# Performance work log

Hardware: AMD Instinct MI355X
Metric: run time of the kernel (lower is better)

Reference implementation:

```python
import jax, jax.numpy as jnp
import numpy as np

N, H, W = 4, 96, 96
C, G, K = 128, 8, 3
GC = C // G          # group channels = 16
P = K * K            # sampling points per group = 9
PAD = K // 2
OFS = 1.0            # offset_scale
HID = 4 * C          # mlp hidden
EPS = 1e-5           # torch nn.LayerNorm default eps


def _ln(x, g, b):
    m = jnp.mean(x, -1, keepdims=True)
    v = jnp.mean((x - m) ** 2, -1, keepdims=True)
    return (x - m) * jax.lax.rsqrt(v + EPS) * g + b


def _dcnv3_core(x, offset, mask):
    # x: (n,H,W,C) channels-last, offset: (n,H,W,G*P*2), mask: (n,H,W,G,P) softmaxed.
    # Faithful port of dcnv3_core_pytorch (stride=1, dilation=1, zero-pad grid_sample,
    # align_corners=False -> pixel = loc*size - 0.5).
    n = x.shape[0]
    xp = jnp.pad(x, ((0, 0), (PAD, PAD), (PAD, PAD), (0, 0)))
    Hin, Win = H + 2 * PAD, W + 2 * PAD
    L = H * W
    base = (K - 1) // 2 + 0.5
    ref_x = (base + jnp.arange(W, dtype=x.dtype)) / Win  # normalized by padded size
    ref_y = (base + jnp.arange(H, dtype=x.dtype)) / Hin
    k = jnp.arange(K, dtype=x.dtype) - (K - 1) // 2
    dx = jnp.repeat(k, K) / Win  # torch meshgrid('ij'): kernel-x varies slowest
    dy = jnp.tile(k, K) / Hin
    off = offset.reshape(n, H, W, G, P, 2)
    # absolute sampling pixel coords (grid_sample align_corners=False)
    px = (ref_x[None, None, :, None, None] + dx * OFS + off[..., 0] * OFS / Win) * Win - 0.5
    py = (ref_y[None, :, None, None, None] + dy * OFS + off[..., 1] * OFS / Hin) * Hin - 0.5
    # layout (n,G,L,P)
    px = px.transpose(0, 3, 1, 2, 4).reshape(n, G, L, P)
    py = py.transpose(0, 3, 1, 2, 4).reshape(n, G, L, P)
    mk = mask.transpose(0, 3, 1, 2, 4).reshape(n, G, L, P)
    xg = xp.reshape(n, Hin * Win, G, GC).transpose(0, 2, 1, 3)
    x0 = jnp.floor(px); y0 = jnp.floor(py)
    fx = px - x0; fy = py - y0
    x0 = x0.astype(jnp.int32); y0 = y0.astype(jnp.int32)
    x1 = x0 + 1; y1 = y0 + 1
    out = jnp.zeros((n, G, L, GC), x.dtype)
    for yi, xi, w in ((y0, x0, (1 - fy) * (1 - fx)), (y0, x1, (1 - fy) * fx),
                      (y1, x0, fy * (1 - fx)), (y1, x1, fy * fx)):
        valid = (yi >= 0) & (yi < Hin) & (xi >= 0) & (xi < Win)
        idx = jnp.clip(yi, 0, Hin - 1) * Win + jnp.clip(xi, 0, Win - 1)
        v = jnp.take_along_axis(xg, idx.reshape(n, G, L * P, 1), axis=2)
        v = v.reshape(n, G, L, P, GC)
        out = out + jnp.einsum('nglp,nglpc->nglc', jnp.where(valid, w, 0.0) * mk, v)
    return out.transpose(0, 2, 1, 3).reshape(n, H, W, C)


def _dcn(x, w_in, b_in, dw_k, dw_b, dwg, dwb, w_off, b_off, w_msk, b_msk, w_out, b_out):
    n = x.shape[0]
    xproj = x @ w_in + b_in
    x1 = jax.lax.conv_general_dilated(
        x, dw_k, (1, 1), 'SAME',
        dimension_numbers=('NHWC', 'HWIO', 'NHWC'),
        feature_group_count=C) + dw_b
    x1 = jax.nn.gelu(_ln(x1, dwg, dwb), approximate=False)
    offset = x1 @ w_off + b_off
    mask = jax.nn.softmax((x1 @ w_msk + b_msk).reshape(n, H, W, G, P), axis=-1)
    y = _dcnv3_core(xproj, offset, mask)
    return y @ w_out + b_out


def setup_inputs() -> dict:
    key = jax.random.key(0)
    ks = jax.random.split(key, 10)
    rn = lambda k, s, sc: jax.random.normal(k, s, jnp.float32) * sc
    return {
        'x': rn(ks[0], (N, H, W, C), 1.0),
        'ln1g': jnp.ones((C,), jnp.float32), 'ln1b': jnp.zeros((C,), jnp.float32),
        'w_in': rn(ks[1], (C, C), 0.02), 'b_in': jnp.zeros((C,), jnp.float32),
        'dw_k': rn(ks[2], (K, K, 1, C), 0.1), 'dw_b': jnp.zeros((C,), jnp.float32),
        'dwg': jnp.ones((C,), jnp.float32), 'dwb': jnp.zeros((C,), jnp.float32),
        'w_off': rn(ks[3], (C, G * P * 2), 0.01), 'b_off': rn(ks[4], (G * P * 2,), 0.1),
        'w_msk': rn(ks[5], (C, G * P), 0.02), 'b_msk': jnp.zeros((G * P,), jnp.float32),
        'w_out': rn(ks[6], (C, C), 0.02), 'b_out': jnp.zeros((C,), jnp.float32),
        'ln2g': jnp.ones((C,), jnp.float32), 'ln2b': jnp.zeros((C,), jnp.float32),
        'w1': rn(ks[7], (C, HID), 0.02), 'b1': jnp.zeros((HID,), jnp.float32),
        'w2': rn(ks[8], (HID, C), 0.02), 'b2': jnp.zeros((C,), jnp.float32),
    }


def reference(x, ln1g, ln1b, w_in, b_in, dw_k, dw_b, dwg, dwb, w_off, b_off,
              w_msk, b_msk, w_out, b_out, ln2g, ln2b, w1, b1, w2, b2):
    # pre-norm InternImage block: x = x + dcn(LN1(x)); x = x + mlp(LN2(x))
    x = x + _dcn(_ln(x, ln1g, ln1b), w_in, b_in, dw_k, dw_b, dwg, dwb,
                 w_off, b_off, w_msk, b_msk, w_out, b_out)
    h = _ln(x, ln2g, ln2b)
    h = jax.nn.gelu(h @ w1 + b1, approximate=False) @ w2 + b2
    return x + h
```

## Files before the change

### kernel.cpp

```cpp
#include <hip/hip_runtime.h>
#include <hip/hip_bf16.h>
#include <math.h>

using bf16 = __hip_bfloat16;
using bf162 = __hip_bfloat162;

typedef __bf16 bf16x8 __attribute__((ext_vector_type(8)));
typedef float floatx4 __attribute__((ext_vector_type(4)));

constexpr int NB = 4, HH = 96, WW = 96, CC = 128, GG = 8, PP = 9;
constexpr int HW = HH * WW;
constexpr int NPIX = NB * HW;

__device__ __forceinline__ float ld1(const float* p) { return *p; }
__device__ __forceinline__ float ld1(const bf16* p)  { return __bfloat162float(*p); }
__device__ __forceinline__ void st1(float* p, float v) { *p = v; }
__device__ __forceinline__ void st1(bf16* p, float v)  { *p = __float2bfloat16(v); }
__device__ __forceinline__ float b2f(bf16 v) { return __bfloat162float(v); }
__device__ __forceinline__ bf16 f2b(float v) { return __float2bfloat16(v); }
__device__ __forceinline__ float gelu_exact(float v) {
    return 0.5f * v * (1.0f + erff(v * 0.7071067811865475f));
}

struct PrepArgs {
    const float* src[6];
    bf16* dst[6];
    int K[6], N[6];
    int cum[7];
};

__global__ __launch_bounds__(256) void prep_weights(PrepArgs pa, int total)
{
    int t = blockIdx.x * 256 + threadIdx.x;
    if (t >= total) return;
    int i = 0;
    #pragma unroll
    for (int j = 0; j < 5; ++j) if (t >= pa.cum[j + 1]) i = j + 1;
    int e = t - pa.cum[i];
    int Ki = pa.K[i], Ni = pa.N[i];
    int n = e / Ki, k = e - n * Ki;
    pa.dst[i][e] = f2b(pa.src[i][(size_t)k * Ni + n]);
}

template<typename TI, typename TO>
__global__ __launch_bounds__(256) void ln_kernel(
    const TI* __restrict__ X, const float* __restrict__ g,
    const float* __restrict__ b, TO* __restrict__ out)
{
    int wave = (blockIdx.x * 256 + threadIdx.x) >> 6;
    int lane = threadIdx.x & 63;
    if (wave >= NPIX) return;
    const TI* xp = X + (size_t)wave * 128 + 2 * lane;
    float v0 = ld1(xp), v1 = ld1(xp + 1);
    float s = v0 + v1, q = v0 * v0 + v1 * v1;
    #pragma unroll
    for (int o = 32; o; o >>= 1) { s += __shfl_xor(s, o); q += __shfl_xor(q, o); }
    float mean = s * (1.0f / 128.0f);
    float rstd = rsqrtf(q * (1.0f / 128.0f) - mean * mean + 1e-5f);
    float g0 = g[2 * lane], g1 = g[2 * lane + 1];
    float b0 = b[2 * lane], b1 = b[2 * lane + 1];
    TO* op = out + (size_t)wave * 128 + 2 * lane;
    st1(op,     (v0 - mean) * rstd * g0 + b0);
    st1(op + 1, (v1 - mean) * rstd * g1 + b1);
}

__global__ __launch_bounds__(256) void dwconv_ln_gelu_kernel(
    const bf16* __restrict__ xln, const float* __restrict__ dwk,
    const float* __restrict__ dwb, const float* __restrict__ gam,
    const float* __restrict__ bet, bf16* __restrict__ out)
{
    int wave = (blockIdx.x * 256 + threadIdx.x) >> 6;
    int lane = threadIdx.x & 63;
    if (wave >= NPIX) return;
    int n = wave / HW; int rem = wave % HW;
    int y = rem / WW;  int x = rem % WW;
    const bf162* xp = (const bf162*)xln;
    float a0 = 0.f, a1 = 0.f;
    #pragma unroll
    for (int ky = 0; ky < 3; ++ky) {
        int yy = y + ky - 1;
        if (yy < 0 || yy >= HH) continue;
        #pragma unroll
        for (int kx = 0; kx < 3; ++kx) {
            int xx = x + kx - 1;
            if (xx < 0 || xx >= WW) continue;
            bf162 v = xp[((size_t)(n * HH + yy) * WW + xx) * 64 + lane];
            const float* w = dwk + (ky * 3 + kx) * CC + 2 * lane;
            a0 = fmaf(b2f(v.x), w[0], a0);
            a1 = fmaf(b2f(v.y), w[1], a1);
        }
    }
    a0 += dwb[2 * lane]; a1 += dwb[2 * lane + 1];
    float s = a0 + a1, q = a0 * a0 + a1 * a1;
    #pragma unroll
    for (int o = 32; o; o >>= 1) { s += __shfl_xor(s, o); q += __shfl_xor(q, o); }
    float mean = s * (1.0f / 128.0f);
    float rstd = rsqrtf(q * (1.0f / 128.0f) - mean * mean + 1e-5f);
    float h0 = gelu_exact((a0 - mean) * rstd * gam[2 * lane]     + bet[2 * lane]);
    float h1 = gelu_exact((a1 - mean) * rstd * gam[2 * lane + 1] + bet[2 * lane + 1]);
    bf162 o2; o2.x = f2b(h0); o2.y = f2b(h1);
    ((bf162*)out)[(size_t)wave * 64 + lane] = o2;
}

__global__ __launch_bounds__(256) void softmax9_kernel(bf16* __restrict__ m)
{
    int t = blockIdx.x * 256 + threadIdx.x;
    if (t >= NPIX * GG) return;
    bf16* p = m + (size_t)t * 9;
    float v[9]; float mx = -1e30f;
    #pragma unroll
    for (int i = 0; i < 9; ++i) { v[i] = b2f(p[i]); mx = fmaxf(mx, v[i]); }
    float s = 0.f;
    #pragma unroll
    for (int i = 0; i < 9; ++i) { v[i] = expf(v[i] - mx); s += v[i]; }
    float r = 1.0f / s;
    #pragma unroll
    for (int i = 0; i < 9; ++i) p[i] = f2b(v[i] * r);
}

__global__ __launch_bounds__(256) void dcn_core_kernel(
    const bf16* __restrict__ xproj, const bf16* __restrict__ off,
    const bf16* __restrict__ msk, bf16* __restrict__ out)
{
    __shared__ int4   sOff[4][72];
    __shared__ float4 sW[4][72];
    int wv = threadIdx.x >> 6;
    int lane = threadIdx.x & 63;
    int pix = blockIdx.x * 4 + wv;
    int n = pix / HW; int rem = pix % HW;
    int iy = rem / WW; int ix = rem % WW;

    for (int e = lane; e < 72; e += 64) {
        int g = e / 9, p = e - 9 * g;
        float ox = b2f(off[(size_t)pix * 144 + g * 18 + 2 * p]);
        float oy = b2f(off[(size_t)pix * 144 + g * 18 + 2 * p + 1]);
        float mw = b2f(msk[(size_t)pix * 72 + e]);
        int kx = p / 3 - 1, ky = p % 3 - 1;
        float px = (float)(ix + kx) + ox;
        float py = (float)(iy + ky) + oy;
        float fx0 = floorf(px), fy0 = floorf(py);
        int x0 = (int)fx0, y0 = (int)fy0;
        float fx = px - fx0, fy = py - fy0;
        bool vx0 = (x0 >= 0) & (x0 < WW), vx1 = (x0 + 1 >= 0) & (x0 + 1 < WW);
        bool vy0 = (y0 >= 0) & (y0 < HH), vy1 = (y0 + 1 >= 0) & (y0 + 1 < HH);
        float w00 = (1.f - fy) * (1.f - fx) * mw * (vy0 && vx0 ? 1.f : 0.f);
        float w01 = (1.f - fy) * fx         * mw * (vy0 && vx1 ? 1.f : 0.f);
        float w10 = fy * (1.f - fx)         * mw * (vy1 && vx0 ? 1.f : 0.f);
        float w11 = fy * fx                 * mw * (vy1 && vx1 ? 1.f : 0.f);
        int x0c = min(max(x0, 0), WW - 1), x1c = min(max(x0 + 1, 0), WW - 1);
        int y0c = min(max(y0, 0), HH - 1), y1c = min(max(y0 + 1, 0), HH - 1);
        sOff[wv][e] = make_int4((y0c * WW + x0c) * CC, (y0c * WW + x1c) * CC,
                                (y1c * WW + x0c) * CC, (y1c * WW + x1c) * CC);
        sW[wv][e] = make_float4(w00, w01, w10, w11);
    }
    __syncthreads();

    const bf16* xb = xproj + (size_t)n * HW * CC + 2 * lane;
    int gbase = (lane >> 3) * 9;
    float a0 = 0.f, a1 = 0.f;
    #pragma unroll
    for (int p = 0; p < 9; ++p) {
        int4 o = sOff[wv][gbase + p];
        float4 w = sW[wv][gbase + p];
        bf162 v00 = *(const bf162*)(xb + o.x);
        bf162 v01 = *(const bf162*)(xb + o.y);
        bf162 v10 = *(const bf162*)(xb + o.z);
        bf162 v11 = *(const bf162*)(xb + o.w);
        a0 += w.x * b2f(v00.x) + w.y * b2f(v01.x) + w.z * b2f(v10.x) + w.w * b2f(v11.x);
        a1 += w.x * b2f(v00.y) + w.y * b2f(v01.y) + w.z * b2f(v10.y) + w.w * b2f(v11.y);
    }
    bf162 o2; o2.x = f2b(a0); o2.y = f2b(a1);
    ((bf162*)out)[(size_t)pix * 64 + lane] = o2;
}

template<typename TR, typename TO>
__global__ __launch_bounds__(256) void gemm_mfma_kernel(
    const bf16* __restrict__ A, const bf16* __restrict__ Wt,
    const float* __restrict__ bias, const TR* __restrict__ R,
    TO* __restrict__ Out, int M, int Nn, int K, int act)
{
    __shared__ __bf16 As[64][72];
    __shared__ __bf16 Bs[64][72];
    int tid = threadIdx.x;
    int wv = tid >> 6, lane = tid & 63;
    int bm = blockIdx.y * 64, bn = blockIdx.x * 64;
    int mI = lane & 15, q = lane >> 4;
    floatx4 acc[4] = {};

    for (int k0 = 0; k0 < K; k0 += 64) {
        #pragma unroll
        for (int cc = 0; cc < 2; ++cc) {
            int ch = tid * 2 + cc;
            int row = ch >> 3, ko = (ch & 7) * 8;
            uint4 av = *reinterpret_cast<const uint4*>(A + (size_t)(bm + row) * K + k0 + ko);
            *reinterpret_cast<uint4*>(&As[row][ko]) = av;
            int ng = bn + row;
            uint4 bv = make_uint4(0, 0, 0, 0);
            if (ng < Nn) bv = *reinterpret_cast<const uint4*>(Wt + (size_t)ng * K + k0 + ko);
            *reinterpret_cast<uint4*>(&Bs[row][ko]) = bv;
        }
        __syncthreads();
        #pragma unroll
        for (int kk = 0; kk < 64; kk += 32) {
            bf16x8 a = *reinterpret_cast<const bf16x8*>(&As[wv * 16 + mI][kk + q * 8]);
            #pragma unroll
            for (int t = 0; t < 4; ++t) {
                bf16x8 b = *reinterpret_cast<const bf16x8*>(&Bs[t * 16 + mI][kk + q * 8]);
                acc[t] = __builtin_amdgcn_mfma_f32_16x16x32_bf16(a, b, acc[t], 0, 0, 0);
            }
        }
        __syncthreads();
    }
    int row0 = bm + wv * 16 + q * 4;
    #pragma unroll
    for (int t = 0; t < 4; ++t) {
        int col = bn + t * 16 + mI;
        if (col >= Nn) continue;
        float bs = bias[col];
        #pragma unroll
        for (int r = 0; r < 4; ++r) {
            int row = row0 + r;
            float v = acc[t][r] + bs;
            if (act == 1) v = gelu_exact(v);
            if (R) v += ld1(R + (size_t)row * Nn + col);
            st1(Out + (size_t)row * Nn + col, v);
        }
    }
}

extern "C" void kernel_launch(void* const* d_in, const int* in_sizes, int n_in,
                              void* d_out, int out_size, void* d_ws, size_t ws_size,
                              hipStream_t stream)
{
    const float* x     = (const float*)d_in[0];
    const float* ln1g  = (const float*)d_in[1];
    const float* ln1b  = (const float*)d_in[2];
    const float* w_in  = (const float*)d_in[3];
    const float* b_in  = (const float*)d_in[4];
    const float* dw_k  = (const float*)d_in[5];
    const float* dw_b  = (const float*)d_in[6];
    const float* dwg   = (const float*)d_in[7];
    const float* dwb   = (const float*)d_in[8];
    const float* w_off = (const float*)d_in[9];
    const float* b_off = (const float*)d_in[10];
    const float* w_msk = (const float*)d_in[11];
    const float* b_msk = (const float*)d_in[12];
    const float* w_out = (const float*)d_in[13];
    const float* b_out = (const float*)d_in[14];
    const float* ln2g  = (const float*)d_in[15];
    const float* ln2b  = (const float*)d_in[16];
    const float* w1    = (const float*)d_in[17];
    const float* b1    = (const float*)d_in[18];
    const float* w2    = (const float*)d_in[19];
    const float* b2    = (const float*)d_in[20];
    float* out = (float*)d_out;

    bf16* ws = (bf16*)d_ws;
    bf16* xln   = ws;
    bf16* xproj = xln   + (size_t)NPIX * 128;
    bf16* x1    = xproj + (size_t)NPIX * 128;
    bf16* mskr  = x1    + (size_t)NPIX * 128;
    bf16* offr  = mskr  + (size_t)NPIX * 72;
    bf16* h1    = offr;
    bf16* ycore = xln;
    bf16* xres  = x1;
    bf16* h2    = xproj;
    bf16* wT    = ws + (size_t)NPIX * 968;
    bf16* w_inT  = wT;
    bf16* w_offT = w_inT  + 16384;
    bf16* w_mskT = w_offT + 18432;
    bf16* w_outT = w_mskT + 9216;
    bf16* w1T    = w_outT + 16384;
    bf16* w2T    = w1T    + 65536;
    const int WTOT = 191488;

    PrepArgs pa;
    pa.src[0] = w_in;  pa.dst[0] = w_inT;  pa.K[0] = 128; pa.N[0] = 128;
    pa.src[1] = w_off; pa.dst[1] = w_offT; pa.K[1] = 128; pa.N[1] = 144;
    pa.src[2] = w_msk; pa.dst[2] = w_mskT; pa.K[2] = 128; pa.N[2] = 72;
    pa.src[3] = w_out; pa.dst[3] = w_outT; pa.K[3] = 128; pa.N[3] = 128;
    pa.src[4] = w1;    pa.dst[4] = w1T;    pa.K[4] = 128; pa.N[4] = 512;
    pa.src[5] = w2;    pa.dst[5] = w2T;    pa.K[5] = 512; pa.N[5] = 128;
    pa.cum[0] = 0;     pa.cum[1] = 16384;  pa.cum[2] = 34816; pa.cum[3] = 44032;
    pa.cum[4] = 60416; pa.cum[5] = 125952; pa.cum[6] = 191488;

    const int M = NPIX;
    dim3 blk(256);

    prep_weights<<<(WTOT + 255) / 256, blk, 0, stream>>>(pa, WTOT);
    ln_kernel<float, bf16><<<NPIX / 4, blk, 0, stream>>>(x, ln1g, ln1b, xln);
    gemm_mfma_kernel<float, bf16><<<dim3(2, M / 64), blk, 0, stream>>>(
        xln, w_inT, b_in, (const float*)nullptr, xproj, M, 128, 128, 0);
    dwconv_ln_gelu_kernel<<<NPIX / 4, blk, 0, stream>>>(xln, dw_k, dw_b, dwg, dwb, x1);
    gemm_mfma_kernel<float, bf16><<<dim3(3, M / 64), blk, 0, stream>>>(
        x1, w_offT, b_off, (const float*)nullptr, offr, M, 144, 128, 0);
    gemm_mfma_kernel<float, bf16><<<dim3(2, M / 64), blk, 0, stream>>>(
        x1, w_mskT, b_msk, (const float*)nullptr, mskr, M, 72, 128, 0);
    softmax9_kernel<<<(NPIX * GG + 255) / 256, blk, 0, stream>>>(mskr);
    dcn_core_kernel<<<NPIX / 4, blk, 0, stream>>>(xproj, offr, mskr, ycore);
    gemm_mfma_kernel<float, bf16><<<dim3(2, M / 64), blk, 0, stream>>>(
        ycore, w_outT, b_out, x, xres, M, 128, 128, 0);
    ln_kernel<bf16, bf16><<<NPIX / 4, blk, 0, stream>>>(xres, ln2g, ln2b, h2);
    gemm_mfma_kernel<float, bf16><<<dim3(8, M / 64), blk, 0, stream>>>(
        h2, w1T, b1, (const float*)nullptr, h1, M, 512, 128, 1);
    gemm_mfma_kernel<bf16, float><<<dim3(2, M / 64), blk, 0, stream>>>(
        h1, w2T, b2, xres, out, M, 128, 512, 0);
}
```

Before: 255.9 us.

## Fuse offset/mask GEMMs, fold softmax into DCN core, enlarge GEMM tiles

Concatenates the offset and mask projection weights and biases so a single GEMM produces both, and removes the separate softmax kernel by computing the 9-way softmax inside the DCN core kernel from shared memory. The GEMM kernel moves from 64x64 to 128x128 block tiles, with each wave computing a 64x64 sub-tile of 4x4 MFMAs. Together these cut kernel launches and intermediate traffic and raise data reuse per block. The trade-off is fewer blocks (about 288 for the N=128 GEMMs), which may leave CUs idle, plus higher register pressure from the 16 accumulators.

```diff
diff --git a/kernel.cpp b/kernel.cpp
--- a/kernel.cpp
+++ b/kernel.cpp
@@ -27,12 +27,18 @@
     bf16* dst[6];
     int K[6], N[6];
     int cum[7];
+    const float* b_off; const float* b_msk; float* b_om;
 };
 
 __global__ __launch_bounds__(256) void prep_weights(PrepArgs pa, int total)
 {
     int t = blockIdx.x * 256 + threadIdx.x;
     if (t >= total) return;
+    if (t >= pa.cum[6]) {
+        int e = t - pa.cum[6];
+        pa.b_om[e] = (e < 144) ? pa.b_off[e] : pa.b_msk[e - 144];
+        return;
+    }
     int i = 0;
     #pragma unroll
     for (int j = 0; j < 5; ++j) if (t >= pa.cum[j + 1]) i = j + 1;
@@ -102,39 +108,36 @@
     ((bf162*)out)[(size_t)wave * 64 + lane] = o2;
 }
 
-__global__ __launch_bounds__(256) void softmax9_kernel(bf16* __restrict__ m)
-{
-    int t = blockIdx.x * 256 + threadIdx.x;
-    if (t >= NPIX * GG) return;
-    bf16* p = m + (size_t)t * 9;
-    float v[9]; float mx = -1e30f;
-    #pragma unroll
-    for (int i = 0; i < 9; ++i) { v[i] = b2f(p[i]); mx = fmaxf(mx, v[i]); }
-    float s = 0.f;
-    #pragma unroll
-    for (int i = 0; i < 9; ++i) { v[i] = expf(v[i] - mx); s += v[i]; }
-    float r = 1.0f / s;
-    #pragma unroll
-    for (int i = 0; i < 9; ++i) p[i] = f2b(v[i] * r);
-}
-
 __global__ __launch_bounds__(256) void dcn_core_kernel(
-    const bf16* __restrict__ xproj, const bf16* __restrict__ off,
-    const bf16* __restrict__ msk, bf16* __restrict__ out)
+    const bf16* __restrict__ xproj, const bf16* __restrict__ omr,
+    bf16* __restrict__ out)
 {
     __shared__ int4   sOff[4][72];
     __shared__ float4 sW[4][72];
+    __shared__ float  sRaw[4][72];
     int wv = threadIdx.x >> 6;
     int lane = threadIdx.x & 63;
     int pix = blockIdx.x * 4 + wv;
     int n = pix / HW; int rem = pix % HW;
     int iy = rem / WW; int ix = rem % WW;
+    const bf16* om = omr + (size_t)pix * 216;
+
+    for (int e = lane; e < 72; e += 64)
+        sRaw[wv][e] = b2f(om[144 + e]);
+    __syncthreads();
 
     for (int e = lane; e < 72; e += 64) {
         int g = e / 9, p = e - 9 * g;
-        float ox = b2f(off[(size_t)pix * 144 + g * 18 + 2 * p]);
-        float oy = b2f(off[(size_t)pix * 144 + g * 18 + 2 * p + 1]);
-        float mw = b2f(msk[(size_t)pix * 72 + e]);
+        float mx = -1e30f;
+        #pragma unroll
+        for (int i = 0; i < 9; ++i) mx = fmaxf(mx, sRaw[wv][g * 9 + i]);
+        float ssum = 0.f;
+        #pragma unroll
+        for (int i = 0; i < 9; ++i) ssum += __expf(sRaw[wv][g * 9 + i] - mx);
+        float mw = __expf(sRaw[wv][e] - mx) / ssum;
+
+        float ox = b2f(om[g * 18 + 2 * p]);
+        float oy = b2f(om[g * 18 + 2 * p + 1]);
         int kx = p / 3 - 1, ky = p % 3 - 1;
         float px = (float)(ix + kx) + ox;
         float py = (float)(iy + ky) + oy;
@@ -179,51 +182,60 @@
     const float* __restrict__ bias, const TR* __restrict__ R,
     TO* __restrict__ Out, int M, int Nn, int K, int act)
 {
-    __shared__ __bf16 As[64][72];
-    __shared__ __bf16 Bs[64][72];
+    __shared__ __bf16 As[128][72];
+    __shared__ __bf16 Bs[128][72];
     int tid = threadIdx.x;
     int wv = tid >> 6, lane = tid & 63;
-    int bm = blockIdx.y * 64, bn = blockIdx.x * 64;
+    int wm = (wv >> 1) * 64, wn = (wv & 1) * 64;
+    int bm = blockIdx.y * 128, bn = blockIdx.x * 128;
     int mI = lane & 15, q = lane >> 4;
-    floatx4 acc[4] = {};
+    floatx4 acc[4][4] = {};
 
     for (int k0 = 0; k0 < K; k0 += 64) {
         #pragma unroll
-        for (int cc = 0; cc < 2; ++cc) {
-            int ch = tid * 2 + cc;
-            int row = ch >> 3, ko = (ch & 7) * 8;
-            uint4 av = *reinterpret_cast<const uint4*>(A + (size_t)(bm + row) * K + k0 + ko);
-            *reinterpret_cast<uint4*>(&As[row][ko]) = av;
-            int ng = bn + row;
-            uint4 bv = make_uint4(0, 0, 0, 0);
-            if (ng < Nn) bv = *reinterpret_cast<const uint4*>(Wt + (size_t)ng * K + k0 + ko);
-            *reinterpret_cast<uint4*>(&Bs[row][ko]) = bv;
+        for (int i = 0; i < 4; ++i) {
+            int s = tid + 256 * i;
+            int row = s >> 3, jp = (s & 7) * 8;
+            *reinterpret_cast<uint4*>(&As[row][jp]) =
+                *reinterpret_cast<const uint4*>(A + (size_t)(bm + row) * K + k0 + jp);
+            int ng = min(bn + row, Nn - 1);
+            *reinterpret_cast<uint4*>(&Bs[row][jp]) =
+                *reinterpret_cast<const uint4*>(Wt + (size_t)ng * K + k0 + jp);
         }
         __syncthreads();
         #pragma unroll
         for (int kk = 0; kk < 64; kk += 32) {
-            bf16x8 a = *reinterpret_cast<const bf16x8*>(&As[wv * 16 + mI][kk + q * 8]);
+            bf16x8 a[4], b[4];
             #pragma unroll
-            for (int t = 0; t < 4; ++t) {
-                bf16x8 b = *reinterpret_cast<const bf16x8*>(&Bs[t * 16 + mI][kk + q * 8]);
-                acc[t] = __builtin_amdgcn_mfma_f32_16x16x32_bf16(a, b, acc[t], 0, 0, 0);
-            }
+            for (int i = 0; i < 4; ++i)
+                a[i] = *reinterpret_cast<const bf16x8*>(&As[wm + i * 16 + mI][kk + q * 8]);
+            #pragma unroll
+            for (int j = 0; j < 4; ++j)
+                b[j] = *reinterpret_cast<const bf16x8*>(&Bs[wn + j * 16 + mI][kk + q * 8]);
+            #pragma unroll
+            for (int i = 0; i < 4; ++i)
+                #pragma unroll
+                for (int j = 0; j < 4; ++j)
+                    acc[i][j] = __builtin_amdgcn_mfma_f32_16x16x32_bf16(a[i], b[j], acc[i][j], 0, 0, 0);
         }
         __syncthreads();
     }
-    int row0 = bm + wv * 16 + q * 4;
-    #pragma unroll
-    for (int t = 0; t < 4; ++t) {
-        int col = bn + t * 16 + mI;
-        if (col >= Nn) continue;
-        float bs = bias[col];
-        #pragma unroll
-        for (int r = 0; r < 4; ++r) {
-            int row = row0 + r;
-            float v = acc[t][r] + bs;
-            if (act == 1) v = gelu_exact(v);
-            if (R) v += ld1(R + (size_t)row * Nn + col);
-            st1(Out + (size_t)row * Nn + col, v);
+    #pragma unroll
+    for (int i = 0; i < 4; ++i) {
+        int row0 = bm + wm + i * 16 + q * 4;
+        #pragma unroll
+        for (int j = 0; j < 4; ++j) {
+            int col = bn + wn + j * 16 + mI;
+            if (col >= Nn) continue;
+            float bs = bias[col];
+            #pragma unroll
+            for (int r = 0; r < 4; ++r) {
+                int row = row0 + r;
+                float v = acc[i][j][r] + bs;
+                if (act == 1) v = gelu_exact(v);
+                if (R) v += ld1(R + (size_t)row * Nn + col);
+                st1(Out + (size_t)row * Nn + col, v);
+            }
         }
     }
 }
@@ -259,50 +271,48 @@
     bf16* xln   = ws;
     bf16* xproj = xln   + (size_t)NPIX * 128;
     bf16* x1    = xproj + (size_t)NPIX * 128;
-    bf16* mskr  = x1    + (size_t)NPIX * 128;
-    bf16* offr  = mskr  + (size_t)NPIX * 72;
-    bf16* h1    = offr;
+    bf16* reg4  = x1    + (size_t)NPIX * 128;
+    bf16* omr   = reg4;
+    bf16* h1    = reg4;
     bf16* ycore = xln;
     bf16* xres  = x1;
     bf16* h2    = xproj;
-    bf16* wT    = ws + (size_t)NPIX * 968;
+    bf16* wT    = ws + (size_t)NPIX * 896;
     bf16* w_inT  = wT;
-    bf16* w_offT = w_inT  + 16384;
-    bf16* w_mskT = w_offT + 18432;
-    bf16* w_outT = w_mskT + 9216;
+    bf16* w_omT  = w_inT  + 16384;
+    bf16* w_outT = w_omT  + 27648;
     bf16* w1T    = w_outT + 16384;
     bf16* w2T    = w1T    + 65536;
-    const int WTOT = 191488;
+    float* b_om  = (float*)(w2T + 65536);
+    const int WTOT = 191488 + 216;
 
     PrepArgs pa;
-    pa.src[0] = w_in;  pa.dst[0] = w_inT;  pa.K[0] = 128; pa.N[0] = 128;
-    pa.src[1] = w_off; pa.dst[1] = w_offT; pa.K[1] = 128; pa.N[1] = 144;
-    pa.src[2] = w_msk; pa.dst[2] = w_mskT; pa.K[2] = 128; pa.N[2] = 72;
-    pa.src[3] = w_out; pa.dst[3] = w_outT; pa.K[3] = 128; pa.N[3] = 128;
-    pa.src[4] = w1;    pa.dst[4] = w1T;    pa.K[4] = 128; pa.N[4] = 512;
-    pa.src[5] = w2;    pa.dst[5] = w2T;    pa.K[5] = 512; pa.N[5] = 128;
+    pa.src[0] = w_in;  pa.dst[0] = w_inT;            pa.K[0] = 128; pa.N[0] = 128;
+    pa.src[1] = w_off; pa.dst[1] = w_omT;            pa.K[1] = 128; pa.N[1] = 144;
+    pa.src[2] = w_msk; pa.dst[2] = w_omT + 144*128;  pa.K[2] = 128; pa.N[2] = 72;
+    pa.src[3] = w_out; pa.dst[3] = w_outT;           pa.K[3] = 128; pa.N[3] = 128;
+    pa.src[4] = w1;    pa.dst[4] = w1T;              pa.K[4] = 128; pa.N[4] = 512;
+    pa.src[5] = w2;    pa.dst[5] = w2T;              pa.K[5] = 512; pa.N[5] = 128;
     pa.cum[0] = 0;     pa.cum[1] = 16384;  pa.cum[2] = 34816; pa.cum[3] = 44032;
     pa.cum[4] = 60416; pa.cum[5] = 125952; pa.cum[6] = 191488;
+    pa.b_off = b_off;  pa.b_msk = b_msk;   pa.b_om = b_om;
 
     const int M = NPIX;
     dim3 blk(256);
 
     prep_weights<<<(WTOT + 255) / 256, blk, 0, stream>>>(pa, WTOT);
     ln_kernel<float, bf16><<<NPIX / 4, blk, 0, stream>>>(x, ln1g, ln1b, xln);
-    gemm_mfma_kernel<float, bf16><<<dim3(2, M / 64), blk, 0, stream>>>(
+    gemm_mfma_kernel<float, bf16><<<dim3(1, M / 128), blk, 0, stream>>>(
         xln, w_inT, b_in, (const float*)nullptr, xproj, M, 128, 128, 0);
     dwconv_ln_gelu_kernel<<<NPIX / 4, blk, 0, stream>>>(xln, dw_k, dw_b, dwg, dwb, x1);
-    gemm_mfma_kernel<float, bf16><<<dim3(3, M / 64), blk, 0, stream>>>(
-        x1, w_offT, b_off, (const float*)nullptr, offr, M, 144, 128, 0);
-    gemm_mfma_kernel<float, bf16><<<dim3(2, M / 64), blk, 0, stream>>>(
-        x1, w_mskT, b_msk, (const float*)nullptr, mskr, M, 72, 128, 0);
-    softmax9_kernel<<<(NPIX * GG + 255) / 256, blk, 0, stream>>>(mskr);
-    dcn_core_kernel<<<NPIX / 4, blk, 0, stream>>>(xproj, offr, mskr, ycore);
-    gemm_mfma_kernel<float, bf16><<<dim3(2, M / 64), blk, 0, stream>>>(
+    gemm_mfma_kernel<float, bf16><<<dim3(2, M / 128), blk, 0, stream>>>(
+        x1, w_omT, b_om, (const float*)nullptr, omr, M, 216, 128, 0);
+    dcn_core_kernel<<<NPIX / 4, blk, 0, stream>>>(xproj, omr, ycore);
+    gemm_mfma_kernel<float, bf16><<<dim3(1, M / 128), blk, 0, stream>>>(
         ycore, w_outT, b_out, x, xres, M, 128, 128, 0);
     ln_kernel<bf16, bf16><<<NPIX / 4, blk, 0, stream>>>(xres, ln2g, ln2b, h2);
-    gemm_mfma_kernel<float, bf16><<<dim3(8, M / 64), blk, 0, stream>>>(
+    gemm_mfma_kernel<float, bf16><<<dim3(4, M / 128), blk, 0, stream>>>(
         h2, w1T, b1, (const float*)nullptr, h1, M, 512, 128, 1);
-    gemm_mfma_kernel<bf16, float><<<dim3(2, M / 64), blk, 0, stream>>>(
+    gemm_mfma_kernel<bf16, float><<<dim3(1, M / 128), blk, 0, stream>>>(
         h1, w2T, b2, xres, out, M, 128, 512, 0);
 }
```

Measured after the change: 305.5 us. 19.3% more time.
